# Performance work log

Measured on AMD Instinct MI355X. Metric: run time of the kernel, lower is better.

Reference implementation:

```python
import jax, jax.numpy as jnp
import numpy as np

H = 2048          # hidden_size
NH = 16           # num query heads
NKV = 8           # num kv heads
HD = 128          # head_dim
T = 4096          # tokens (single causal prefill sequence)
THETA = 1000000.0
EPS = 1e-6
QS = NH * HD
KVS = NKV * HD
SCALE = HD ** -0.5


def setup_inputs() -> dict:
    key = jax.random.key(0)
    k0, k1, k2 = jax.random.split(key, 3)
    return {
        "positions": jnp.arange(T, dtype=jnp.int32),
        "hidden_states": jax.random.normal(k0, (T, H), jnp.float32),
        "w_qkv": jax.random.normal(k1, (H, QS + 2 * KVS), jnp.float32) * 0.02,
        "w_o": jax.random.normal(k2, (QS, H), jnp.float32) * 0.02,
        "q_norm_w": jnp.ones((HD,), jnp.float32),
        "k_norm_w": jnp.ones((HD,), jnp.float32),
    }


def _rmsnorm(x, w):
    # per-head RMSNorm over last dim (head_dim)
    return x * jax.lax.rsqrt(jnp.mean(x * x, axis=-1, keepdims=True) + EPS) * w


def _rope(x, cos, sin):
    # neox-style rotate-half RoPE; x: [T, nheads, HD], cos/sin: [T, 1, HD/2]
    x1, x2 = jnp.split(x, 2, axis=-1)
    return jnp.concatenate([x1 * cos - x2 * sin, x2 * cos + x1 * sin], axis=-1)


def reference(positions, hidden_states, w_qkv, w_o, q_norm_w, k_norm_w):
    # fused QKV projection then split
    qkv = hidden_states @ w_qkv                      # [T, QS+2*KVS]
    q, k, v = jnp.split(qkv, [QS, QS + KVS], axis=-1)
    q = _rmsnorm(q.reshape(T, NH, HD), q_norm_w)     # per-head QK RMSNorm
    k = _rmsnorm(k.reshape(T, NKV, HD), k_norm_w)
    v = v.reshape(T, NKV, HD)

    # RoPE over full head_dim
    inv_freq = 1.0 / (THETA ** (jnp.arange(0, HD, 2, dtype=jnp.float32) / HD))
    ang = positions.astype(jnp.float32)[:, None] * inv_freq  # [T, HD/2]
    cos = jnp.cos(ang)[:, None, :]
    sin = jnp.sin(ang)[:, None, :]
    q = _rope(q, cos, sin)
    k = _rope(k, cos, sin)

    # causal GQA attention (prefill path of RadixAttention)
    G = NH // NKV
    q4 = q.reshape(T, NKV, G, HD) * SCALE
    scores = jnp.einsum('tkgd,skd->kgts', q4, k)     # [NKV, G, T, T]
    causal = jnp.tril(jnp.ones((T, T), dtype=bool))
    scores = jnp.where(causal, scores, jnp.float32(-1e30))
    probs = jax.nn.softmax(scores, axis=-1)
    out = jnp.einsum('kgts,skd->tkgd', probs, v).reshape(T, QS)
    return out @ w_o
```

## Files before the change

### kernel.cpp

```cpp
#include <hip/hip_runtime.h>
#include <hip/hip_bf16.h>
#include <math.h>

#define T_TOK 4096
#define H_DIM 2048
#define NH 16
#define NKV 8
#define HD 128
#define QS (NH * HD)
#define KVS (NKV * HD)
#define QKV_W (QS + 2*KVS)
#define QSCALE (0.08838834764831845f * 1.4426950408889634f)
#define EPS 1e-6f

typedef short short8 __attribute__((ext_vector_type(8)));
typedef short short4v __attribute__((ext_vector_type(4)));
typedef float floatx4 __attribute__((ext_vector_type(4)));

#if __has_builtin(__builtin_amdgcn_exp2f)
#define EXP2(x) __builtin_amdgcn_exp2f(x)
#else
#define EXP2(x) exp2f(x)
#endif

__device__ __forceinline__ unsigned short f2bf(float f) {
    unsigned int u = __float_as_uint(f);
    unsigned int r = (u + 0x7FFFu + ((u >> 16) & 1u)) >> 16;
    return (unsigned short)r;
}
__device__ __forceinline__ float bf2f(unsigned short u) {
    unsigned int v = ((unsigned int)u) << 16;
    return __uint_as_float(v);
}
__device__ __forceinline__ unsigned int pk2(float a, float b) {
    union { __hip_bfloat162 h; unsigned int u; } c;
    c.h = __float22bfloat162_rn(make_float2(a, b));
    return c.u;
}

__device__ __forceinline__ void gload_lds16(const unsigned short* g, unsigned short* l) {
    __builtin_amdgcn_global_load_lds(
        (const __attribute__((address_space(1))) unsigned int*)(const void*)g,
        (__attribute__((address_space(3))) unsigned int*)(void*)l, 16, 0, 0);
}

__global__ __launch_bounds__(256) void cvt_bf16(const float* __restrict__ in,
                                                unsigned short* __restrict__ out) {
    int idx = (blockIdx.x * 256 + threadIdx.x) * 8;
    float4 v0 = *(const float4*)&in[idx];
    float4 v1 = *(const float4*)&in[idx + 4];
    short8 t;
    t[0] = (short)f2bf(v0.x); t[1] = (short)f2bf(v0.y);
    t[2] = (short)f2bf(v0.z); t[3] = (short)f2bf(v0.w);
    t[4] = (short)f2bf(v1.x); t[5] = (short)f2bf(v1.y);
    t[6] = (short)f2bf(v1.z); t[7] = (short)f2bf(v1.w);
    *(short8*)&out[idx] = t;
}

__global__ __launch_bounds__(256) void cvt_transpose(const float* __restrict__ in,
                                                     unsigned short* __restrict__ out,
                                                     int K, int N) {
    __shared__ __align__(16) unsigned short t[64][72];
    const int tid = threadIdx.x;
    const int n0 = blockIdx.x * 64, k0 = blockIdx.y * 64;
    const int r = tid >> 4, c4 = (tid & 15) * 4;
    #pragma unroll
    for (int i = 0; i < 4; ++i) {
        int kk = r + 16 * i;
        float4 v = *(const float4*)&in[(size_t)(k0 + kk) * N + n0 + c4];
        t[c4 + 0][kk] = f2bf(v.x); t[c4 + 1][kk] = f2bf(v.y);
        t[c4 + 2][kk] = f2bf(v.z); t[c4 + 3][kk] = f2bf(v.w);
    }
    __syncthreads();
    const int n = tid >> 2, c8 = (tid & 3) * 16;
    short8 a = *(const short8*)&t[n][c8];
    short8 b = *(const short8*)&t[n][c8 + 8];
    *(short8*)&out[(size_t)(n0 + n) * K + k0 + c8] = a;
    *(short8*)&out[(size_t)(n0 + n) * K + k0 + c8 + 8] = b;
}

template<bool C_BF16>
__global__ __launch_bounds__(256) void gemm_bt(const unsigned short* __restrict__ A, int lda,
                                               const unsigned short* __restrict__ Bt, int ldb,
                                               void* __restrict__ Cptr, int ldc, int K) {
    __shared__ __align__(16) unsigned short As[128 * 32];
    __shared__ __align__(16) unsigned short Bs[128 * 32];
    const int tid = threadIdx.x;
    const int wave = tid >> 6, lane = tid & 63;
    const int quad = lane >> 4, l16 = lane & 15;
    const int wm = wave >> 1, wn = wave & 1;
    const int bm = blockIdx.y * 128, bn = blockIdx.x * 128;

    floatx4 acc[4][4] = {};
    for (int k0 = 0; k0 < K; k0 += 32) {
        #pragma unroll
        for (int i = 0; i < 2; ++i) {
            int c = wave * 128 + i * 64 + lane;
            int row = c >> 2, off = (c & 3) * 8;
            gload_lds16(A  + (size_t)(bm + row) * lda + k0 + off, As + (size_t)(wave * 128 + i * 64) * 8);
            gload_lds16(Bt + (size_t)(bn + row) * ldb + k0 + off, Bs + (size_t)(wave * 128 + i * 64) * 8);
        }
        __syncthreads();
        short8 a[4], b[4];
        #pragma unroll
        for (int mi = 0; mi < 4; ++mi)
            a[mi] = *(const short8*)&As[(wm * 64 + mi * 16 + l16) * 32 + quad * 8];
        #pragma unroll
        for (int ni = 0; ni < 4; ++ni)
            b[ni] = *(const short8*)&Bs[(wn * 64 + ni * 16 + l16) * 32 + quad * 8];
        #pragma unroll
        for (int mi = 0; mi < 4; ++mi)
            #pragma unroll
            for (int ni = 0; ni < 4; ++ni)
                acc[mi][ni] = __builtin_amdgcn_mfma_f32_16x16x32_bf16(a[mi], b[ni], acc[mi][ni], 0, 0, 0);
        __syncthreads();
    }
    #pragma unroll
    for (int mi = 0; mi < 4; ++mi)
        #pragma unroll
        for (int ni = 0; ni < 4; ++ni)
            #pragma unroll
            for (int r = 0; r < 4; ++r) {
                int row = bm + wm * 64 + mi * 16 + quad * 4 + r;
                int col = bn + wn * 64 + ni * 16 + l16;
                if (C_BF16)
                    ((unsigned short*)Cptr)[(size_t)row * ldc + col] = f2bf(acc[mi][ni][r]);
                else
                    ((float*)Cptr)[(size_t)row * ldc + col] = acc[mi][ni][r];
            }
}

template<bool C_BF16>
__global__ __launch_bounds__(512, 2) void gemm256(const unsigned short* __restrict__ A, int lda,
                                                  const unsigned short* __restrict__ Bt, int ldb,
                                                  void* __restrict__ Cptr, int ldc, int K, int nbx) {
    __shared__ __align__(16) unsigned short lds[4 * 16384];
    const int tid  = threadIdx.x;
    const int wave = tid >> 6, lane = tid & 63;
    const int quad = lane >> 4, l16 = lane & 15;
    const int wm = wave >> 2, wn = wave & 3;

    const int cpx = gridDim.x >> 3;
    const int swz = (blockIdx.x & 7) * cpx + (blockIdx.x >> 3);
    const int by = swz / nbx, bx = swz % nbx;
    const int bm = by * 256, bn = bx * 256;

    const int ch0 = wave * 64 + lane;
    const int ch1 = 512 + ch0;
    const int ar0 = ch0 >> 2, ac0 = ((ch0 & 3) ^ (ar0 & 3)) * 8;
    const int ar1 = ch1 >> 2, ac1 = ((ch1 & 3) ^ (ar1 & 3)) * 8;
    const unsigned short* a0 = A  + (size_t)(bm + ar0) * lda + ac0;
    const unsigned short* a1 = A  + (size_t)(bm + ar1) * lda + ac1;
    const unsigned short* b0 = Bt + (size_t)(bn + ar0) * ldb + ac0;
    const unsigned short* b1 = Bt + (size_t)(bn + ar1) * ldb + ac1;
    const unsigned du0 = (unsigned)(wave * 64) * 8;
    const unsigned du1 = (unsigned)(512 + wave * 64) * 8;

    auto stage = [&](int kofs, int sb) {
        gload_lds16(a0 + kofs, &lds[sb + du0]);
        gload_lds16(a1 + kofs, &lds[sb + du1]);
        gload_lds16(b0 + kofs, &lds[sb + 8192 + du0]);
        gload_lds16(b1 + kofs, &lds[sb + 8192 + du1]);
    };

    floatx4 acc[8][4] = {};
    const int arow = wm * 128 + l16;
    const int brow = wn * 64 + l16;
    const int sslot = (quad ^ (l16 & 3)) * 8;

    auto compute = [&](int cbo) {
        short8 bfr[4];
        #pragma unroll
        for (int ni = 0; ni < 4; ++ni)
            bfr[ni] = *(const short8*)&lds[cbo + 8192 + (brow + ni * 16) * 32 + sslot];
        __builtin_amdgcn_s_setprio(1);
        #pragma unroll
        for (int mi = 0; mi < 8; ++mi) {
            short8 afr = *(const short8*)&lds[cbo + (arow + mi * 16) * 32 + sslot];
            #pragma unroll
            for (int ni = 0; ni < 4; ++ni)
                acc[mi][ni] = __builtin_amdgcn_mfma_f32_16x16x32_bf16(afr, bfr[ni], acc[mi][ni], 0, 0, 0);
        }
        __builtin_amdgcn_s_setprio(0);
    };

    const int NT = K >> 5;
    stage(0,  0);
    stage(32, 16384);
    stage(64, 32768);

    int cb = 0;
    for (int t = 0; t < NT - 3; ++t) {
        stage((t + 3) * 32, (cb + 3 * 16384) & 65535);
        asm volatile("s_waitcnt vmcnt(12)" ::: "memory");
        __builtin_amdgcn_s_barrier();
        asm volatile("" ::: "memory");
        compute(cb);
        asm volatile("" ::: "memory");
        __builtin_amdgcn_s_barrier();
        cb = (cb + 16384) & 65535;
    }
    asm volatile("s_waitcnt vmcnt(8)" ::: "memory");
    __builtin_amdgcn_s_barrier();
    asm volatile("" ::: "memory");
    compute(cb);
    asm volatile("" ::: "memory");
    __builtin_amdgcn_s_barrier();
    cb = (cb + 16384) & 65535;

    asm volatile("s_waitcnt vmcnt(4)" ::: "memory");
    __builtin_amdgcn_s_barrier();
    asm volatile("" ::: "memory");
    compute(cb);
    asm volatile("" ::: "memory");
    __builtin_amdgcn_s_barrier();
    cb = (cb + 16384) & 65535;

    asm volatile("s_waitcnt vmcnt(0)" ::: "memory");
    __builtin_amdgcn_s_barrier();
    asm volatile("" ::: "memory");
    compute(cb);

    #pragma unroll
    for (int mi = 0; mi < 8; ++mi)
        #pragma unroll
        for (int ni = 0; ni < 4; ++ni)
            #pragma unroll
            for (int r = 0; r < 4; ++r) {
                int row = bm + wm * 128 + mi * 16 + quad * 4 + r;
                int col = bn + wn * 64 + ni * 16 + l16;
                if (C_BF16)
                    ((unsigned short*)Cptr)[(size_t)row * ldc + col] = f2bf(acc[mi][ni][r]);
                else
                    ((float*)Cptr)[(size_t)row * ldc + col] = acc[mi][ni][r];
            }
}

__global__ __launch_bounds__(256) void rms_rope_bf16(unsigned short* __restrict__ qkv,
                                                     const int* __restrict__ positions,
                                                     const float* __restrict__ qw,
                                                     const float* __restrict__ kw) {
    const int t = blockIdx.x;
    const int wave = threadIdx.x >> 6;
    const int lane = threadIdx.x & 63;
    const float pos = (float)positions[t];
    unsigned short* row = qkv + (size_t)t * QKV_W;
    const float inv_freq = powf(1000000.0f, -(float)lane / 64.0f);
    float sv, cv;
    sincosf(pos * inv_freq, &sv, &cv);
    for (int h = wave; h < NH + NKV; h += 4) {
        unsigned short* x = row + h * HD;
        const float* w = (h < NH) ? qw : kw;
        const float hs = (h < NH) ? QSCALE : 1.0f;
        float x1 = bf2f(x[lane]);
        float x2 = bf2f(x[lane + 64]);
        float ss = x1 * x1 + x2 * x2;
        #pragma unroll
        for (int off = 32; off > 0; off >>= 1) ss += __shfl_xor(ss, off, 64);
        float r = rsqrtf(ss * (1.0f / 128.0f) + EPS) * hs;
        float n1 = x1 * r * w[lane];
        float n2 = x2 * r * w[lane + 64];
        x[lane]      = f2bf(n1 * cv - n2 * sv);
        x[lane + 64] = f2bf(n2 * cv + n1 * sv);
    }
}

__global__ __launch_bounds__(256) void kv_pack(const unsigned short* __restrict__ qkv,
                                               unsigned short* __restrict__ Kp,
                                               unsigned short* __restrict__ Vp) {
    const int tile = blockIdx.x, kvh = blockIdx.y, tid = threadIdx.x;
    const int t0 = tile * 128;
    const size_t tb = (size_t)(kvh * 32 + tile) * 16384;
    #pragma unroll
    for (int i = 0; i < 8; ++i) {
        int cid = i * 256 + tid;
        int s = cid >> 4, c = cid & 15;
        short8 v = *(const short8*)&qkv[(size_t)(t0 + s) * QKV_W + QS + kvh * HD + c * 8];
        *(short8*)&Kp[tb + (s * 16 + (c ^ (s & 7))) * 8] = v;
    }
    __shared__ __align__(16) unsigned short Lt[128 * 136];
    #pragma unroll
    for (int i = 0; i < 8; ++i) {
        int cid = i * 256 + tid;
        int s = cid >> 4, c = cid & 15;
        short8 v = *(const short8*)&qkv[(size_t)(t0 + s) * QKV_W + QS + KVS + kvh * HD + c * 8];
        #pragma unroll
        for (int e = 0; e < 8; ++e)
            Lt[(c * 8 + e) * 136 + s] = (unsigned short)v[e];
    }
    __syncthreads();
    #pragma unroll
    for (int i = 0; i < 8; ++i) {
        int cid = i * 256 + tid;
        int d = cid >> 4, cs = cid & 15;
        short8 v = *(const short8*)&Lt[d * 136 + cs * 8];
        short8 w;
        if ((d >> 3) & 1) {
            #pragma unroll
            for (int e = 0; e < 8; ++e) w[e] = v[e ^ 4];
        } else w = v;
        *(short8*)&Vp[tb + (d * 16 + (cs ^ (d & 7))) * 8] = w;
    }
}

__global__ __launch_bounds__(256, 2) void attn_mfma(unsigned short* __restrict__ qkv,
                                                    const unsigned short* __restrict__ Kp,
                                                    const unsigned short* __restrict__ Vp) {
    __shared__ __align__(16) unsigned short Ks[128 * 128];
    __shared__ __align__(16) unsigned short Vs[128 * 128];
    const int bx = blockIdx.x;
    const int h = bx & 15, kvh = h >> 1;
    const int g = bx >> 4;
    const int qt = (g < 16) ? (31 - g) : (g - 16);
    const int tid = threadIdx.x;
    const int wave = tid >> 6, lane = tid & 63;
    const int quad = lane >> 4, l16 = lane & 15;
    const int t0 = qt * 128;
    const int wrow0 = t0 + wave * 32;
    const int swz = l16 & 7;
    const int hsel = (l16 >> 3) & 1;
    const int vhalf = ((quad & 1) ^ hsel) * 4;
    const int q2 = quad >> 1;

    short8 qf[2][4];
    #pragma unroll
    for (int rt = 0; rt < 2; ++rt)
        #pragma unroll
        for (int ks = 0; ks < 4; ++ks) {
            int rowg = t0 + wave * 32 + rt * 16 + l16;
            qf[rt][ks] = *(const short8*)&qkv[(size_t)rowg * QKV_W + h * HD + ks * 32 + quad * 8];
        }

    float l_s[2] = {};
    floatx4 oacc[2][8] = {};

    for (int st = 0; st <= qt; ++st) {
        const int s0 = st * 128;
        const unsigned short* kb = Kp + (size_t)(kvh * 32 + st) * 16384;
        const unsigned short* vb = Vp + (size_t)(kvh * 32 + st) * 16384;
        #pragma unroll
        for (int i = 0; i < 8; ++i) {
            int ch = i * 256 + tid;
            gload_lds16(kb + (size_t)ch * 8, Ks + (i * 256 + wave * 64) * 8);
        }
        #pragma unroll
        for (int i = 0; i < 8; ++i) {
            int ch = i * 256 + tid;
            gload_lds16(vb + (size_t)ch * 8, Vs + (i * 256 + wave * 64) * 8);
        }
        __syncthreads();

        const bool diag = (st == qt);
        #pragma unroll
        for (int ct = 0; ct < 8; ++ct) {
            const int smin = s0 + ct * 16;
            if (diag && smin > wrow0 + 31) continue;
            floatx4 sacc[2] = {};
            #pragma unroll
            for (int ks = 0; ks < 4; ++ks) {
                short8 kfr = *(const short8*)&Ks[(ct * 16 + l16) * 128 + ((ks * 4 + quad) ^ swz) * 8];
                sacc[0] = __builtin_amdgcn_mfma_f32_16x16x32_bf16(kfr, qf[0][ks], sacc[0], 0, 0, 0);
                sacc[1] = __builtin_amdgcn_mfma_f32_16x16x32_bf16(kfr, qf[1][ks], sacc[1], 0, 0, 0);
            }
            short4v pp[2];
            #pragma unroll
            for (int rt = 0; rt < 2; ++rt) {
                const int tg = wrow0 + rt * 16 + l16;
                float p[4];
                float lsum = 0.0f;
                #pragma unroll
                for (int r = 0; r < 4; ++r) {
                    float s = sacc[rt][r];
                    if (diag && (smin + quad * 4 + r > tg)) s = -1e30f;
                    p[r] = EXP2(s);
                    lsum += p[r];
                }
                l_s[rt] += lsum;
                union { short4v s4; unsigned int u[2]; } pk;
                pk.u[0] = pk2(p[0], p[1]);
                pk.u[1] = pk2(p[2], p[3]);
                pp[rt] = pk.s4;
            }
            const int vc = (((ct * 2 + q2) ^ swz)) * 8 + vhalf;
#if __has_builtin(__builtin_amdgcn_mfma_f32_16x16x16bf16_1k)
            #pragma unroll
            for (int dct = 0; dct < 8; ++dct) {
                short4v bfr = *(const short4v*)&Vs[(dct * 16 + l16) * 128 + vc];
                oacc[0][dct] = __builtin_amdgcn_mfma_f32_16x16x16bf16_1k(pp[0], bfr, oacc[0][dct], 0, 0, 0);
                oacc[1][dct] = __builtin_amdgcn_mfma_f32_16x16x16bf16_1k(pp[1], bfr, oacc[1][dct], 0, 0, 0);
            }
#else
            #pragma unroll
            for (int dct = 0; dct < 8; ++dct) {
                union { short8 s8; short4v s4[2]; } b;
                b.s4[0] = *(const short4v*)&Vs[(dct * 16 + l16) * 128 + vc];
                b.s4[1] = short4v{0, 0, 0, 0};
                #pragma unroll
                for (int rt = 0; rt < 2; ++rt) {
                    union { short8 s8; short4v s4[2]; } a;
                    a.s4[0] = pp[rt];
                    a.s4[1] = short4v{0, 0, 0, 0};
                    oacc[rt][dct] = __builtin_amdgcn_mfma_f32_16x16x32_bf16(a.s8, b.s8, oacc[rt][dct], 0, 0, 0);
                }
            }
#endif
        }
        __syncthreads();
    }

    float lred[2];
    #pragma unroll
    for (int rt = 0; rt < 2; ++rt) {
        float l = l_s[rt];
        l += __shfl_xor(l, 16, 64);
        l += __shfl_xor(l, 32, 64);
        lred[rt] = l;
    }
    #pragma unroll
    for (int rt = 0; rt < 2; ++rt)
        #pragma unroll
        for (int r = 0; r < 4; ++r) {
            float l = __shfl(lred[rt], quad * 4 + r, 64);
            float linv = 1.0f / l;
            int rowg = t0 + wave * 32 + rt * 16 + quad * 4 + r;
            #pragma unroll
            for (int dct = 0; dct < 8; ++dct)
                qkv[(size_t)rowg * QKV_W + h * HD + dct * 16 + l16] = f2bf(oacc[rt][dct][r] * linv);
        }
}

extern "C" void kernel_launch(void* const* d_in, const int* in_sizes, int n_in,
                              void* d_out, int out_size, void* d_ws, size_t ws_size,
                              hipStream_t stream) {
    const int*   positions = (const int*)d_in[0];
    const float* hidden    = (const float*)d_in[1];
    const float* w_qkv     = (const float*)d_in[2];
    const float* w_o       = (const float*)d_in[3];
    const float* q_norm_w  = (const float*)d_in[4];
    const float* k_norm_w  = (const float*)d_in[5];
    float* out = (float*)d_out;

    unsigned short* qkvb   = (unsigned short*)d_ws;
    unsigned short* h_bf   = (unsigned short*)((char*)d_ws + ((size_t)32 << 20));
    unsigned short* Kp     = (unsigned short*)((char*)d_ws + ((size_t)32 << 20));
    unsigned short* Vp     = (unsigned short*)((char*)d_ws + ((size_t)40 << 20));
    unsigned short* wqkv_t = (unsigned short*)((char*)d_ws + ((size_t)48 << 20));
    unsigned short* wo_t   = (unsigned short*)((char*)d_ws + ((size_t)48 << 20));

    cvt_bf16<<<(T_TOK * H_DIM) / (256 * 8), 256, 0, stream>>>(hidden, h_bf);
    cvt_transpose<<<dim3(QKV_W / 64, H_DIM / 64), 256, 0, stream>>>(w_qkv, wqkv_t, H_DIM, QKV_W);
    gemm256<true><<<dim3(256), 512, 0, stream>>>(
        h_bf, H_DIM, wqkv_t, H_DIM, qkvb, QKV_W, H_DIM, QKV_W / 256);
    rms_rope_bf16<<<T_TOK, 256, 0, stream>>>(qkvb, positions, q_norm_w, k_norm_w);
    kv_pack<<<dim3(T_TOK / 128, NKV), 256, 0, stream>>>(qkvb, Kp, Vp);
    cvt_transpose<<<dim3(H_DIM / 64, QS / 64), 256, 0, stream>>>(w_o, wo_t, QS, H_DIM);
    attn_mfma<<<512, 256, 0, stream>>>(qkvb, Kp, Vp);
    gemm_bt<false><<<dim3(H_DIM / 128, T_TOK / 128), 256, 0, stream>>>(
        qkvb, QKV_W, wo_t, QS, out, H_DIM, QS);
}
```

Before: 380.5 us.

## Split attention query tile across eight waves and stagger V transpose writes

```diff
diff --git a/kernel.cpp b/kernel.cpp
--- a/kernel.cpp
+++ b/kernel.cpp
@@ -245,7 +245,7 @@
     const int lane = threadIdx.x & 63;
     const float pos = (float)positions[t];
     unsigned short* row = qkv + (size_t)t * QKV_W;
-    const float inv_freq = powf(1000000.0f, -(float)lane / 64.0f);
+    const float inv_freq = exp2f(-(float)lane * (19.931568569324174f / 64.0f));
     float sv, cv;
     sincosf(pos * inv_freq, &sv, &cv);
     for (int h = wave; h < NH + NKV; h += 4) {
@@ -285,8 +285,10 @@
         int s = cid >> 4, c = cid & 15;
         short8 v = *(const short8*)&qkv[(size_t)(t0 + s) * QKV_W + QS + KVS + kvh * HD + c * 8];
         #pragma unroll
-        for (int e = 0; e < 8; ++e)
-            Lt[(c * 8 + e) * 136 + s] = (unsigned short)v[e];
+        for (int e = 0; e < 8; ++e) {
+            int ee = (e + c) & 7;
+            Lt[(c * 8 + ee) * 136 + s] = (unsigned short)v[ee];
+        }
     }
     __syncthreads();
     #pragma unroll
@@ -303,7 +305,7 @@
     }
 }
 
-__global__ __launch_bounds__(256, 2) void attn_mfma(unsigned short* __restrict__ qkv,
+__global__ __launch_bounds__(512, 4) void attn_mfma(unsigned short* __restrict__ qkv,
                                                     const unsigned short* __restrict__ Kp,
                                                     const unsigned short* __restrict__ Vp) {
     __shared__ __align__(16) unsigned short Ks[128 * 128];
@@ -316,37 +318,35 @@
     const int wave = tid >> 6, lane = tid & 63;
     const int quad = lane >> 4, l16 = lane & 15;
     const int t0 = qt * 128;
-    const int wrow0 = t0 + wave * 32;
+    const int wrow0 = t0 + wave * 16;
     const int swz = l16 & 7;
     const int hsel = (l16 >> 3) & 1;
     const int vhalf = ((quad & 1) ^ hsel) * 4;
     const int q2 = quad >> 1;
 
-    short8 qf[2][4];
-    #pragma unroll
-    for (int rt = 0; rt < 2; ++rt)
-        #pragma unroll
-        for (int ks = 0; ks < 4; ++ks) {
-            int rowg = t0 + wave * 32 + rt * 16 + l16;
-            qf[rt][ks] = *(const short8*)&qkv[(size_t)rowg * QKV_W + h * HD + ks * 32 + quad * 8];
-        }
-
-    float l_s[2] = {};
-    floatx4 oacc[2][8] = {};
+    short8 qf[4];
+    #pragma unroll
+    for (int ks = 0; ks < 4; ++ks) {
+        int rowg = wrow0 + l16;
+        qf[ks] = *(const short8*)&qkv[(size_t)rowg * QKV_W + h * HD + ks * 32 + quad * 8];
+    }
+
+    float l_s = 0.0f;
+    floatx4 oacc[8] = {};
 
     for (int st = 0; st <= qt; ++st) {
         const int s0 = st * 128;
         const unsigned short* kb = Kp + (size_t)(kvh * 32 + st) * 16384;
         const unsigned short* vb = Vp + (size_t)(kvh * 32 + st) * 16384;
         #pragma unroll
-        for (int i = 0; i < 8; ++i) {
-            int ch = i * 256 + tid;
-            gload_lds16(kb + (size_t)ch * 8, Ks + (i * 256 + wave * 64) * 8);
-        }
-        #pragma unroll
-        for (int i = 0; i < 8; ++i) {
-            int ch = i * 256 + tid;
-            gload_lds16(vb + (size_t)ch * 8, Vs + (i * 256 + wave * 64) * 8);
+        for (int i = 0; i < 4; ++i) {
+            int ch = i * 512 + tid;
+            gload_lds16(kb + (size_t)ch * 8, Ks + (i * 512 + wave * 64) * 8);
+        }
+        #pragma unroll
+        for (int i = 0; i < 4; ++i) {
+            int ch = i * 512 + tid;
+            gload_lds16(vb + (size_t)ch * 8, Vs + (i * 512 + wave * 64) * 8);
         }
         __syncthreads();
 
@@ -354,40 +354,34 @@
         #pragma unroll
         for (int ct = 0; ct < 8; ++ct) {
             const int smin = s0 + ct * 16;
-            if (diag && smin > wrow0 + 31) continue;
-            floatx4 sacc[2] = {};
+            if (diag && smin > wrow0 + 15) continue;
+            floatx4 sacc = {};
             #pragma unroll
             for (int ks = 0; ks < 4; ++ks) {
                 short8 kfr = *(const short8*)&Ks[(ct * 16 + l16) * 128 + ((ks * 4 + quad) ^ swz) * 8];
-                sacc[0] = __builtin_amdgcn_mfma_f32_16x16x32_bf16(kfr, qf[0][ks], sacc[0], 0, 0, 0);
-                sacc[1] = __builtin_amdgcn_mfma_f32_16x16x32_bf16(kfr, qf[1][ks], sacc[1], 0, 0, 0);
-            }
-            short4v pp[2];
-            #pragma unroll
-            for (int rt = 0; rt < 2; ++rt) {
-                const int tg = wrow0 + rt * 16 + l16;
-                float p[4];
-                float lsum = 0.0f;
-                #pragma unroll
-                for (int r = 0; r < 4; ++r) {
-                    float s = sacc[rt][r];
-                    if (diag && (smin + quad * 4 + r > tg)) s = -1e30f;
-                    p[r] = EXP2(s);
-                    lsum += p[r];
-                }
-                l_s[rt] += lsum;
-                union { short4v s4; unsigned int u[2]; } pk;
-                pk.u[0] = pk2(p[0], p[1]);
-                pk.u[1] = pk2(p[2], p[3]);
-                pp[rt] = pk.s4;
-            }
+                sacc = __builtin_amdgcn_mfma_f32_16x16x32_bf16(kfr, qf[ks], sacc, 0, 0, 0);
+            }
+            const int tg = wrow0 + l16;
+            float p[4];
+            float lsum = 0.0f;
+            #pragma unroll
+            for (int r = 0; r < 4; ++r) {
+                float s = sacc[r];
+                if (diag && (smin + quad * 4 + r > tg)) s = -1e30f;
+                p[r] = EXP2(s);
+                lsum += p[r];
+            }
+            l_s += lsum;
+            union { short4v s4; unsigned int u[2]; } pk;
+            pk.u[0] = pk2(p[0], p[1]);
+            pk.u[1] = pk2(p[2], p[3]);
+            short4v pp = pk.s4;
             const int vc = (((ct * 2 + q2) ^ swz)) * 8 + vhalf;
 #if __has_builtin(__builtin_amdgcn_mfma_f32_16x16x16bf16_1k)
             #pragma unroll
             for (int dct = 0; dct < 8; ++dct) {
                 short4v bfr = *(const short4v*)&Vs[(dct * 16 + l16) * 128 + vc];
-                oacc[0][dct] = __builtin_amdgcn_mfma_f32_16x16x16bf16_1k(pp[0], bfr, oacc[0][dct], 0, 0, 0);
-                oacc[1][dct] = __builtin_amdgcn_mfma_f32_16x16x16bf16_1k(pp[1], bfr, oacc[1][dct], 0, 0, 0);
+                oacc[dct] = __builtin_amdgcn_mfma_f32_16x16x16bf16_1k(pp, bfr, oacc[dct], 0, 0, 0);
             }
 #else
             #pragma unroll
@@ -395,38 +389,28 @@
                 union { short8 s8; short4v s4[2]; } b;
                 b.s4[0] = *(const short4v*)&Vs[(dct * 16 + l16) * 128 + vc];
                 b.s4[1] = short4v{0, 0, 0, 0};
-                #pragma unroll
-                for (int rt = 0; rt < 2; ++rt) {
-                    union { short8 s8; short4v s4[2]; } a;
-                    a.s4[0] = pp[rt];
-                    a.s4[1] = short4v{0, 0, 0, 0};
-                    oacc[rt][dct] = __builtin_amdgcn_mfma_f32_16x16x32_bf16(a.s8, b.s8, oacc[rt][dct], 0, 0, 0);
-                }
+                union { short8 s8; short4v s4[2]; } a;
+                a.s4[0] = pp;
+                a.s4[1] = short4v{0, 0, 0, 0};
+                oacc[dct] = __builtin_amdgcn_mfma_f32_16x16x32_bf16(a.s8, b.s8, oacc[dct], 0, 0, 0);
             }
 #endif
         }
         __syncthreads();
     }
 
-    float lred[2];
-    #pragma unroll
-    for (int rt = 0; rt < 2; ++rt) {
-        float l = l_s[rt];
-        l += __shfl_xor(l, 16, 64);
-        l += __shfl_xor(l, 32, 64);
-        lred[rt] = l;
-    }
-    #pragma unroll
-    for (int rt = 0; rt < 2; ++rt)
-        #pragma unroll
-        for (int r = 0; r < 4; ++r) {
-            float l = __shfl(lred[rt], quad * 4 + r, 64);
-            float linv = 1.0f / l;
-            int rowg = t0 + wave * 32 + rt * 16 + quad * 4 + r;
-            #pragma unroll
-            for (int dct = 0; dct < 8; ++dct)
-                qkv[(size_t)rowg * QKV_W + h * HD + dct * 16 + l16] = f2bf(oacc[rt][dct][r] * linv);
-        }
+    float lred = l_s;
+    lred += __shfl_xor(lred, 16, 64);
+    lred += __shfl_xor(lred, 32, 64);
+    #pragma unroll
+    for (int r = 0; r < 4; ++r) {
+        float l = __shfl(lred, quad * 4 + r, 64);
+        float linv = 1.0f / l;
+        int rowg = wrow0 + quad * 4 + r;
+        #pragma unroll
+        for (int dct = 0; dct < 8; ++dct)
+            qkv[(size_t)rowg * QKV_W + h * HD + dct * 16 + l16] = f2bf(oacc[dct][r] * linv);
+    }
 }
 
 extern "C" void kernel_launch(void* const* d_in, const int* in_sizes, int n_in,
@@ -454,7 +438,7 @@
     rms_rope_bf16<<<T_TOK, 256, 0, stream>>>(qkvb, positions, q_norm_w, k_norm_w);
     kv_pack<<<dim3(T_TOK / 128, NKV), 256, 0, stream>>>(qkvb, Kp, Vp);
     cvt_transpose<<<dim3(H_DIM / 64, QS / 64), 256, 0, stream>>>(w_o, wo_t, QS, H_DIM);
-    attn_mfma<<<512, 256, 0, stream>>>(qkvb, Kp, Vp);
+    attn_mfma<<<512, 512, 0, stream>>>(qkvb, Kp, Vp);
     gemm_bt<false><<<dim3(H_DIM / 128, T_TOK / 128), 256, 0, stream>>>(
         qkvb, QKV_W, wo_t, QS, out, H_DIM, QS);
 }
```

New measurement: 387.2 us. No clear change (+1.7%).
